# Kernel optimization log

Measured on AMD Instinct MI355X. Metric: run time of the kernel, lower is better.

## Reference

```python
import jax, jax.numpy as jnp
import numpy as np

NUM_HEADS = 16

def setup_inputs() -> dict:
    key = jax.random.key(0)
    k1, k2, k3 = jax.random.split(key, 3)
    B, S, D = 4, 2048, 1024
    x = jax.random.normal(k1, (B, S, D), dtype=jnp.float32)
    w_qkv = jax.random.normal(k2, (D, 3 * D), dtype=jnp.float32) * (1.0 / np.sqrt(D))
    b_qkv = jnp.zeros((3 * D,), dtype=jnp.float32)
    w_out = jax.random.normal(k3, (D, D), dtype=jnp.float32) * (1.0 / np.sqrt(D))
    b_out = jnp.zeros((D,), dtype=jnp.float32)
    return {"x": x, "w_qkv": w_qkv, "b_qkv": b_qkv, "w_out": w_out, "b_out": b_out}

def reference(x, w_qkv, b_qkv, w_out, b_out):
    B, S, D = x.shape
    H = NUM_HEADS
    Dh = D // H
    # fused QKV projection: [B,S,3D]
    qkv = jnp.einsum('bsd,de->bse', x, w_qkv) + b_qkv
    q, k, v = jnp.split(qkv, 3, axis=-1)
    # separate heads -> [B,H,S,Dh]
    def heads(t):
        return t.reshape(B, S, H, Dh).transpose(0, 2, 1, 3)
    q, k, v = heads(q), heads(k), heads(v)
    # scaled dot-product attention (no mask, no dropout)
    scale = 1.0 / jnp.sqrt(jnp.asarray(Dh, dtype=x.dtype))
    attn = jnp.einsum('bhqd,bhkd->bhqk', q, k) * scale
    weights = jax.nn.softmax(attn, axis=-1)
    out = jnp.einsum('bhqk,bhkd->bhqd', weights, v)
    # combine heads -> [B,S,D], then output projection
    out = out.transpose(0, 2, 1, 3).reshape(B, S, D)
    return jnp.einsum('bsd,de->bse', out, w_out) + b_out
```

## Files before the change

### kernel.cpp

```cpp
#include <hip/hip_runtime.h>

typedef unsigned short u16;
typedef __attribute__((ext_vector_type(8))) short v8s;
typedef __attribute__((ext_vector_type(4))) short v4s;
typedef __attribute__((ext_vector_type(4))) float v4f;
typedef __attribute__((ext_vector_type(2))) unsigned int v2u;

#define MFMA32(a, b, c) __builtin_amdgcn_mfma_f32_16x16x32_bf16(a, b, c, 0, 0, 0)

#if __has_builtin(__builtin_amdgcn_exp2f)
#define EXP2(x) __builtin_amdgcn_exp2f(x)
#else
#define EXP2(x) exp2f(x)
#endif

#if __has_builtin(__builtin_amdgcn_mfma_f32_16x16x16bf16_1k)
static __device__ __forceinline__ v4f mfma16(v4s a, v4s b, v4f c) {
    return __builtin_amdgcn_mfma_f32_16x16x16bf16_1k(a, b, c, 0, 0, 0);
}
#else
static __device__ __forceinline__ v4f mfma16(v4s a, v4s b, v4f c) {
    v4s z = {0, 0, 0, 0};
    v8s a8 = __builtin_shufflevector(a, z, 0, 1, 2, 3, 4, 5, 6, 7);
    v8s b8 = __builtin_shufflevector(b, z, 0, 1, 2, 3, 4, 5, 6, 7);
    return MFMA32(a8, b8, c);
}
#endif

static __device__ __forceinline__ u16 f32_to_bf16(float f) {
    unsigned int u = __builtin_bit_cast(unsigned int, f);
    u += 0x7fffu + ((u >> 16) & 1u);
    return (u16)(u >> 16);
}
static __device__ __forceinline__ v8s cvt8(v4f lo, v4f hi) {
    v8s r;
#pragma unroll
    for (int i = 0; i < 4; i++) {
        r[i]     = (short)f32_to_bf16(lo[i]);
        r[i + 4] = (short)f32_to_bf16(hi[i]);
    }
    return r;
}

static __device__ __forceinline__ v4s pack4(float a, float b, float c, float d) {
    const unsigned int ua = __builtin_bit_cast(unsigned int, a) + 0x8000u;
    const unsigned int ub = __builtin_bit_cast(unsigned int, b) + 0x8000u;
    const unsigned int uc = __builtin_bit_cast(unsigned int, c) + 0x8000u;
    const unsigned int ud = __builtin_bit_cast(unsigned int, d) + 0x8000u;
    v2u t = {__builtin_amdgcn_perm(ub, ua, 0x07060302u),
             __builtin_amdgcn_perm(ud, uc, 0x07060302u)};
    return __builtin_bit_cast(v4s, t);
}

__global__ void cast_f32_bf16(const float* __restrict__ in,
                              u16* __restrict__ out, int n8) {
    const int i = blockIdx.x * blockDim.x + threadIdx.x;
    if (i < n8) {
        v4f lo = ((const v4f*)in)[2 * i];
        v4f hi = ((const v4f*)in)[2 * i + 1];
        ((v8s*)out)[i] = cvt8(lo, hi);
    }
}

__global__ void transpose_f32_bf16(const float* __restrict__ in,
                                   u16* __restrict__ out, int R, int C) {
    __shared__ u16 t[32][33];
    const int tid = threadIdx.x;
    const int tx = tid & 31, ty = tid >> 5;
    const int c0 = blockIdx.x * 32, r0 = blockIdx.y * 32;
#pragma unroll
    for (int i = 0; i < 32; i += 8)
        t[ty + i][tx] = f32_to_bf16(in[(size_t)(r0 + ty + i) * C + c0 + tx]);
    __syncthreads();
#pragma unroll
    for (int i = 0; i < 32; i += 8)
        out[(size_t)(c0 + ty + i) * R + r0 + tx] = t[tx][ty + i];
}

template <int AMODE, int CMODE>
__global__ __launch_bounds__(256)
void gemm_bt(const void* __restrict__ A, int lda,
             const u16* __restrict__ Bt, int ldb,
             const float* __restrict__ bias,
             void* __restrict__ Cq, u16* __restrict__ Kb, u16* __restrict__ VtG,
             int ldc, int K) {
    __shared__ __align__(16) u16 As[128 * 72];
    __shared__ __align__(16) u16 Bs[128 * 72];

    const int tid  = threadIdx.x;
    const int wid  = tid >> 6;
    const int lane = tid & 63;
    const int l15  = lane & 15;
    const int quad = lane >> 4;
    const int bm = blockIdx.y * 128;
    const int bn = blockIdx.x * 128;
    const int wm = (wid & 1) * 64;
    const int wn = (wid >> 1) * 64;

    const int sr = tid >> 3;
    const int sg = (tid & 7) * 8;

    const float* Af = (const float*)A;
    const u16*   Au = (const u16*)A;

    v4f acc[4][4];
#pragma unroll
    for (int i = 0; i < 4; i++)
#pragma unroll
        for (int j = 0; j < 4; j++) acc[i][j] = (v4f)0.f;

    for (int kb = 0; kb < K; kb += 64) {
        v8s a[4], b[4];
#pragma unroll
        for (int i = 0; i < 4; i++) {
            const int row = sr + i * 32;
            if (AMODE) {
                const float* p = Af + (size_t)(bm + row) * lda + kb + sg;
                a[i] = cvt8(*(const v4f*)p, *(const v4f*)(p + 4));
            } else {
                a[i] = *(const v8s*)(Au + (size_t)(bm + row) * lda + kb + sg);
            }
            b[i] = *(const v8s*)(Bt + (size_t)(bn + row) * ldb + kb + sg);
        }
        __syncthreads();
#pragma unroll
        for (int i = 0; i < 4; i++) {
            const int row = sr + i * 32;
            *(v8s*)&As[row * 72 + sg] = a[i];
            *(v8s*)&Bs[row * 72 + sg] = b[i];
        }
        __syncthreads();

        v8s af[2][4], bf[2][4];
#pragma unroll
        for (int ko = 0; ko < 2; ko++) {
#pragma unroll
            for (int mt = 0; mt < 4; mt++)
                af[ko][mt] = *(const v8s*)&As[(wm + mt * 16 + l15) * 72 + ko * 32 + quad * 8];
#pragma unroll
            for (int nt = 0; nt < 4; nt++)
                bf[ko][nt] = *(const v8s*)&Bs[(wn + nt * 16 + l15) * 72 + ko * 32 + quad * 8];
        }
#pragma unroll
        for (int ko = 0; ko < 2; ko++)
#pragma unroll
            for (int mt = 0; mt < 4; mt++)
#pragma unroll
                for (int nt = 0; nt < 4; nt++)
                    acc[mt][nt] = MFMA32(af[ko][mt], bf[ko][nt], acc[mt][nt]);
    }

#pragma unroll
    for (int nt = 0; nt < 4; nt++) {
        const int n = bn + wn + nt * 16 + l15;
        const float bv = bias[n];
#pragma unroll
        for (int mt = 0; mt < 4; mt++) {
#pragma unroll
            for (int r = 0; r < 4; r++) {
                const int m = bm + wm + mt * 16 + quad * 4 + r;
                const float val = acc[mt][nt][r] + bv;
                if (CMODE == 1) {
                    ((float*)Cq)[(size_t)m * ldc + n] = val;
                } else {
                    const int region = n >> 10, nl = n & 1023;
                    const float sv = (region == 0) ? val * 0.18033688f : val;
                    const u16 o = f32_to_bf16(sv);
                    if (region == 0) {
                        ((u16*)Cq)[(size_t)m * 1024 + nl] = o;
                    } else if (region == 1) {
                        Kb[(size_t)m * 1024 + nl] = o;
                    } else {
                        const int h = nl >> 6, dh = nl & 63;
                        const int b = m >> 11, s = m & 2047;
                        VtG[((size_t)((b * 16 + h) * 64 + dh)) * 2048 + s] = o;
                    }
                }
            }
        }
    }
}

__global__ __launch_bounds__(256)
void attn_fused(u16* __restrict__ Qb, const u16* __restrict__ Kb,
                const u16* __restrict__ VtG) {
    __shared__ __align__(16) u16 Ks[64 * 72];
    __shared__ __align__(16) u16 Vs[64 * 72];

    const int tid  = threadIdx.x;
    const int wid  = tid >> 6;
    const int lane = tid & 63;
    const int l15  = lane & 15;
    const int quad = lane >> 4;
    const int qt = blockIdx.x;
    const int h  = blockIdx.y;
    const int bz = blockIdx.z;

    const size_t qbase = (size_t)bz * 2048 * 1024;
    const int q0 = qt * 128 + wid * 32;

    v8s aq[2][2];
#pragma unroll
    for (int qh = 0; qh < 2; qh++) {
        const u16* qrow = Qb + qbase + (size_t)(q0 + qh * 16 + l15) * 1024 + h * 64 + quad * 8;
        aq[qh][0] = *(const v8s*)qrow;
        aq[qh][1] = *(const v8s*)(qrow + 32);
    }

    v4f accO[2][4];
    v4f accL[2];
#pragma unroll
    for (int qh = 0; qh < 2; qh++) {
        accL[qh] = (v4f)0.f;
#pragma unroll
        for (int c = 0; c < 4; c++) accO[qh][c] = (v4f)0.f;
    }
    const v4s ones = {(short)0x3F80, (short)0x3F80, (short)0x3F80, (short)0x3F80};

    const int sr = tid >> 3;
    const int sg = (tid & 7) * 8;

    const u16* kpb = Kb + qbase + h * 64;
    const u16* vpb = VtG + (size_t)((bz * 16 + h) * 64) * 2048;

    for (int kt = 0; kt < 32; kt++) {
        const v8s k0 = *(const v8s*)(kpb + (size_t)(kt * 64 + sr) * 1024 + sg);
        const v8s k1 = *(const v8s*)(kpb + (size_t)(kt * 64 + sr + 32) * 1024 + sg);
        const v8s v0 = *(const v8s*)(vpb + (size_t)sr * 2048 + kt * 64 + sg);
        const v8s v1 = *(const v8s*)(vpb + (size_t)(sr + 32) * 2048 + kt * 64 + sg);
        __syncthreads();
        *(v8s*)&Ks[sr * 72 + sg]        = k0;
        *(v8s*)&Ks[(sr + 32) * 72 + sg] = k1;
        *(v8s*)&Vs[sr * 72 + sg]        = v0;
        *(v8s*)&Vs[(sr + 32) * 72 + sg] = v1;
        __syncthreads();

#pragma unroll
        for (int kc = 0; kc < 4; kc++) {
            const v8s kf0 = *(const v8s*)&Ks[(kc * 16 + l15) * 72 + quad * 8];
            const v8s kf1 = *(const v8s*)&Ks[(kc * 16 + l15) * 72 + 32 + quad * 8];
            v4s vf[4];
#pragma unroll
            for (int c = 0; c < 4; c++)
                vf[c] = *(const v4s*)&Vs[(c * 16 + l15) * 72 + kc * 16 + quad * 4];

#pragma unroll
            for (int qh = 0; qh < 2; qh++) {
                v4f st = (v4f)0.f;
                st = MFMA32(kf0, aq[qh][0], st);
                st = MFMA32(kf1, aq[qh][1], st);
                const float p0 = EXP2(st[0]);
                const float p1 = EXP2(st[1]);
                const float p2 = EXP2(st[2]);
                const float p3 = EXP2(st[3]);
                const v4s pk = pack4(p0, p1, p2, p3);
                accL[qh] = mfma16(ones, pk, accL[qh]);
#pragma unroll
                for (int c = 0; c < 4; c++)
                    accO[qh][c] = mfma16(vf[c], pk, accO[qh][c]);
            }
        }
    }

#pragma unroll
    for (int qh = 0; qh < 2; qh++) {
        const int q = q0 + qh * 16 + l15;
        const float inv = 1.f / accL[qh][0];
#pragma unroll
        for (int c = 0; c < 4; c++) {
            const v4s o = pack4(accO[qh][c][0] * inv, accO[qh][c][1] * inv,
                                accO[qh][c][2] * inv, accO[qh][c][3] * inv);
            *(v4s*)&Qb[qbase + (size_t)q * 1024 + h * 64 + c * 16 + quad * 4] = o;
        }
    }
}

extern "C" void kernel_launch(void* const* d_in, const int* in_sizes, int n_in,
                              void* d_out, int out_size, void* d_ws, size_t ws_size,
                              hipStream_t stream) {
    (void)in_sizes; (void)n_in; (void)out_size;
    const float* x    = (const float*)d_in[0];
    const float* wqkv = (const float*)d_in[1];
    const float* bqkv = (const float*)d_in[2];
    const float* wout = (const float*)d_in[3];
    const float* bout = (const float*)d_in[4];
    float* outp = (float*)d_out;

    char* ws = (char*)d_ws;
    const size_t BIG  = 58720256;
    const size_t BIGX = 75497472;

    if (ws_size >= BIG || ws_size == 0) {
        u16* Qb    = (u16*)(ws);
        u16* Kb    = (u16*)(ws + 16777216);
        u16* VtG   = (u16*)(ws + 33554432);
        u16* wqkvT = (u16*)(ws + 50331648);
        u16* woutT = (u16*)(ws + 56623104);
        u16* xb    = (u16*)(ws + 58720256);

        transpose_f32_bf16<<<dim3(96, 32), 256, 0, stream>>>(wqkv, wqkvT, 1024, 3072);
        transpose_f32_bf16<<<dim3(32, 32), 256, 0, stream>>>(wout, woutT, 1024, 1024);
        if (ws_size >= BIGX) {
            cast_f32_bf16<<<4096, 256, 0, stream>>>(x, xb, 1048576);
            gemm_bt<0, 2><<<dim3(24, 64), 256, 0, stream>>>(
                xb, 1024, wqkvT, 1024, bqkv, Qb, Kb, VtG, 0, 1024);
        } else {
            gemm_bt<1, 2><<<dim3(24, 64), 256, 0, stream>>>(
                x, 1024, wqkvT, 1024, bqkv, Qb, Kb, VtG, 0, 1024);
        }
        attn_fused<<<dim3(16, 16, 4), 256, 0, stream>>>(Qb, Kb, VtG);
        gemm_bt<0, 1><<<dim3(8, 64), 256, 0, stream>>>(
            Qb, 1024, woutT, 1024, bout, outp, nullptr, nullptr, 1024, 1024);
    } else {
        u16* wqkvT = (u16*)(ws);
        u16* woutT = (u16*)(ws + 6291456);
        u16* Qb    = (u16*)(ws + 8388608);
        u16* Kb    = (u16*)(ws + 12582912);
        u16* VtG   = (u16*)(ws + 16777216);

        transpose_f32_bf16<<<dim3(96, 32), 256, 0, stream>>>(wqkv, wqkvT, 1024, 3072);
        transpose_f32_bf16<<<dim3(32, 32), 256, 0, stream>>>(wout, woutT, 1024, 1024);
        for (int b = 0; b < 4; b++) {
            const float* xb = x + (size_t)b * 2048 * 1024;
            float* ob = outp + (size_t)b * 2048 * 1024;
            gemm_bt<1, 2><<<dim3(24, 16), 256, 0, stream>>>(
                xb, 1024, wqkvT, 1024, bqkv, Qb, Kb, VtG, 0, 1024);
            attn_fused<<<dim3(16, 16, 1), 256, 0, stream>>>(Qb, Kb, VtG);
            gemm_bt<0, 1><<<dim3(8, 16), 256, 0, stream>>>(
                Qb, 1024, woutT, 1024, bout, ob, nullptr, nullptr, 1024, 1024);
        }
    }
}
```

Measured before the change: 318.8 us.

## Add global_load_lds GEMM and stage bf16 x in output buffer

Adds a new 128x128 bf16 GEMM kernel that loads A and B tiles directly from global memory into LDS with global_load_lds, skipping the register round trip. It replaces the old gemm_bt for both the QKV projection and the output projection. The bf16 copy of x is now always made and written into the output buffer instead of extra workspace, so the cast path runs even when workspace is small. The LDS tiles are unpadded and there is no double buffering, so LDS bank conflicts and exposed load latency may remain.

```diff
diff --git a/kernel.cpp b/kernel.cpp
--- a/kernel.cpp
+++ b/kernel.cpp
@@ -50,6 +50,12 @@
     v2u t = {__builtin_amdgcn_perm(ub, ua, 0x07060302u),
              __builtin_amdgcn_perm(ud, uc, 0x07060302u)};
     return __builtin_bit_cast(v4s, t);
+}
+
+static __device__ __forceinline__ void gld16(const u16* g, u16* l) {
+    __builtin_amdgcn_global_load_lds(
+        (const __attribute__((address_space(1))) void*)g,
+        (__attribute__((address_space(3))) void*)l, 16, 0, 0);
 }
 
 __global__ void cast_f32_bf16(const float* __restrict__ in,
@@ -181,6 +187,95 @@
     }
 }
 
+template <int CMODE>
+__global__ __launch_bounds__(256)
+void gemm_gld(const u16* __restrict__ A, int lda,
+              const u16* __restrict__ Bt, int ldb,
+              const float* __restrict__ bias,
+              void* __restrict__ Cq, u16* __restrict__ Kb, u16* __restrict__ VtG,
+              int ldc, int K) {
+    __shared__ __align__(16) u16 As[128 * 64];
+    __shared__ __align__(16) u16 Bs[128 * 64];
+
+    const int tid  = threadIdx.x;
+    const int wid  = tid >> 6;
+    const int lane = tid & 63;
+    const int l15  = lane & 15;
+    const int quad = lane >> 4;
+    const int bm = blockIdx.y * 128;
+    const int bn = blockIdx.x * 128;
+    const int wm = (wid & 1) * 64;
+    const int wn = (wid >> 1) * 64;
+
+    const int srow = lane >> 3;
+    const int scol = (lane & 7) * 8;
+
+    v4f acc[4][4];
+#pragma unroll
+    for (int i = 0; i < 4; i++)
+#pragma unroll
+        for (int j = 0; j < 4; j++) acc[i][j] = (v4f)0.f;
+
+    for (int kb = 0; kb < K; kb += 64) {
+        __syncthreads();
+#pragma unroll
+        for (int r = 0; r < 4; r++) {
+            const int row0 = r * 32 + wid * 8;
+            gld16(A  + (size_t)(bm + row0 + srow) * lda + kb + scol, &As[row0 * 64]);
+            gld16(Bt + (size_t)(bn + row0 + srow) * ldb + kb + scol, &Bs[row0 * 64]);
+        }
+        __syncthreads();
+
+        v8s af[2][4], bf[2][4];
+#pragma unroll
+        for (int ko = 0; ko < 2; ko++) {
+#pragma unroll
+            for (int mt = 0; mt < 4; mt++)
+                af[ko][mt] = *(const v8s*)&As[(wm + mt * 16 + l15) * 64 + ko * 32 + quad * 8];
+#pragma unroll
+            for (int nt = 0; nt < 4; nt++)
+                bf[ko][nt] = *(const v8s*)&Bs[(wn + nt * 16 + l15) * 64 + ko * 32 + quad * 8];
+        }
+#pragma unroll
+        for (int ko = 0; ko < 2; ko++)
+#pragma unroll
+            for (int mt = 0; mt < 4; mt++)
+#pragma unroll
+                for (int nt = 0; nt < 4; nt++)
+                    acc[mt][nt] = MFMA32(af[ko][mt], bf[ko][nt], acc[mt][nt]);
+    }
+
+#pragma unroll
+    for (int nt = 0; nt < 4; nt++) {
+        const int n = bn + wn + nt * 16 + l15;
+        const float bv = bias[n];
+#pragma unroll
+        for (int mt = 0; mt < 4; mt++) {
+#pragma unroll
+            for (int r = 0; r < 4; r++) {
+                const int m = bm + wm + mt * 16 + quad * 4 + r;
+                const float val = acc[mt][nt][r] + bv;
+                if (CMODE == 1) {
+                    ((float*)Cq)[(size_t)m * ldc + n] = val;
+                } else {
+                    const int region = n >> 10, nl = n & 1023;
+                    const float sv = (region == 0) ? val * 0.18033688f : val;
+                    const u16 o = f32_to_bf16(sv);
+                    if (region == 0) {
+                        ((u16*)Cq)[(size_t)m * 1024 + nl] = o;
+                    } else if (region == 1) {
+                        Kb[(size_t)m * 1024 + nl] = o;
+                    } else {
+                        const int h = nl >> 6, dh = nl & 63;
+                        const int b = m >> 11, s = m & 2047;
+                        VtG[((size_t)((b * 16 + h) * 64 + dh)) * 2048 + s] = o;
+                    }
+                }
+            }
+        }
+    }
+}
+
 __global__ __launch_bounds__(256)
 void attn_fused(u16* __restrict__ Qb, const u16* __restrict__ Kb,
                 const u16* __restrict__ VtG) {
@@ -288,7 +383,6 @@
 
     char* ws = (char*)d_ws;
     const size_t BIG  = 58720256;
-    const size_t BIGX = 75497472;
 
     if (ws_size >= BIG || ws_size == 0) {
         u16* Qb    = (u16*)(ws);
@@ -296,20 +390,15 @@
         u16* VtG   = (u16*)(ws + 33554432);
         u16* wqkvT = (u16*)(ws + 50331648);
         u16* woutT = (u16*)(ws + 56623104);
-        u16* xb    = (u16*)(ws + 58720256);
+        u16* xb    = (u16*)outp;
 
         transpose_f32_bf16<<<dim3(96, 32), 256, 0, stream>>>(wqkv, wqkvT, 1024, 3072);
         transpose_f32_bf16<<<dim3(32, 32), 256, 0, stream>>>(wout, woutT, 1024, 1024);
-        if (ws_size >= BIGX) {
-            cast_f32_bf16<<<4096, 256, 0, stream>>>(x, xb, 1048576);
-            gemm_bt<0, 2><<<dim3(24, 64), 256, 0, stream>>>(
-                xb, 1024, wqkvT, 1024, bqkv, Qb, Kb, VtG, 0, 1024);
-        } else {
-            gemm_bt<1, 2><<<dim3(24, 64), 256, 0, stream>>>(
-                x, 1024, wqkvT, 1024, bqkv, Qb, Kb, VtG, 0, 1024);
-        }
+        cast_f32_bf16<<<4096, 256, 0, stream>>>(x, xb, 1048576);
+        gemm_gld<2><<<dim3(24, 64), 256, 0, stream>>>(
+            xb, 1024, wqkvT, 1024, bqkv, Qb, Kb, VtG, 0, 1024);
         attn_fused<<<dim3(16, 16, 4), 256, 0, stream>>>(Qb, Kb, VtG);
-        gemm_bt<0, 1><<<dim3(8, 64), 256, 0, stream>>>(
+        gemm_gld<1><<<dim3(8, 64), 256, 0, stream>>>(
             Qb, 1024, woutT, 1024, bout, outp, nullptr, nullptr, 1024, 1024);
     } else {
         u16* wqkvT = (u16*)(ws);
```

After: 327.4 us. 1.03x slower.
